# Kernel optimization log

Measured on AMD Instinct MI355X. Metric: run time of the kernel, lower is better.

Reference implementation:

```python
import jax, jax.numpy as jnp
import numpy as np

B, Q, DIM, HEADS, HEAD_DIM, KV = 32, 4, 2048, 16, 128, 8192


def setup_inputs() -> dict:
    key = jax.random.key(0)
    ks = jax.random.split(key, 9)
    s = 0.02
    return {
        'x': jax.random.normal(ks[0], (B, Q, DIM), jnp.float32),
        'attn_bias': jax.random.normal(ks[1], (B, HEADS, Q, KV), jnp.float32),
        'cache_k': jax.random.normal(ks[2], (B, KV, HEAD_DIM), jnp.float32),
        'cache_v': jax.random.normal(ks[3], (B, KV, HEAD_DIM), jnp.float32),
        'wq': jax.random.normal(ks[4], (DIM, HEADS, HEAD_DIM), jnp.float32) * s,
        'bq': jnp.zeros((HEADS, HEAD_DIM), jnp.float32),
        'wk': jax.random.normal(ks[5], (DIM, HEAD_DIM), jnp.float32) * s,
        'bk': jnp.zeros((HEAD_DIM,), jnp.float32),
        'wv': jax.random.normal(ks[6], (DIM, HEAD_DIM), jnp.float32) * s,
        'bv': jnp.zeros((HEAD_DIM,), jnp.float32),
        'wo': jax.random.normal(ks[7], (HEADS, HEAD_DIM, DIM), jnp.float32) * s,
        'bo': jnp.zeros((DIM,), jnp.float32),
    }


def reference(x, attn_bias, cache_k, cache_v, wq, bq, wk, bk, wv, bv, wo, bo):
    q_len = x.shape[1]
    # projections (MQA: shared single-head K/V)
    q = jnp.einsum('bqd,dhe->bqhe', x, wq) + bq          # [B,Q,H,hd]
    k_new = x @ wk + bk                                   # [B,Q,hd]
    v_new = x @ wv + bv
    # rolling KV cache update: shift left by q_len, write new tokens at end
    k = jnp.roll(cache_k, -q_len, axis=1).at[:, -q_len:].set(k_new)  # [B,KV,hd]
    v = jnp.roll(cache_v, -q_len, axis=1).at[:, -q_len:].set(v_new)
    scale = 1.0 / (k.shape[-1] ** 0.5)
    p = jnp.einsum('bqhe,bke->bhqk', q, k) * scale        # [B,H,Q,KV]
    a = jax.nn.softmax(p + attn_bias, axis=-1)
    o = jnp.einsum('bhqk,bke->bqhe', a, v)                # [B,Q,H,hd]
    return jnp.einsum('bqhe,hed->bqd', o, wo) + bo        # [B,Q,DIM]
```

## Files before the change

### kernel.cpp

```cpp
#include <hip/hip_runtime.h>
#include <cstddef>
#include <cstdint>

#define BATCH 32
#define QL 4
#define DIM 2048
#define NH 16
#define HD 128
#define KVLEN 8192
#define HQ 64
#define CHUNK 256
#define NCKB 32
#define NCK 16
#define KT 64
#define NT 4

typedef __attribute__((ext_vector_type(8))) short bf16x8;
typedef __attribute__((ext_vector_type(4))) float f32x4;

__device__ __forceinline__ unsigned short cvt_bf16(float f) {
    unsigned int u = __builtin_bit_cast(unsigned int, f);
    u += 0x7fffu + ((u >> 16) & 1u);
    return (unsigned short)(u >> 16);
}
__device__ __forceinline__ unsigned int pack2(float a, float b) {
    return (unsigned int)cvt_bf16(a) | ((unsigned int)cvt_bf16(b) << 16);
}
__device__ __forceinline__ float bf16_to_f32(unsigned short s) {
    unsigned int u = ((unsigned int)s) << 16;
    return __builtin_bit_cast(float, u);
}
__device__ __forceinline__ bf16x8 mk_frag(unsigned int a, unsigned int b,
                                          unsigned int c, unsigned int d) {
    unsigned int t[4] = {a, b, c, d};
    return *(const bf16x8*)t;
}

template<int VARIANT>
__global__ __launch_bounds__(256) void gemm_kernel(
    const float* __restrict__ A,
    const float* __restrict__ w0p, const float* __restrict__ w1p,
    const float* __restrict__ w2p,
    const float* __restrict__ b0p, const float* __restrict__ b1p,
    const float* __restrict__ b2p,
    float* __restrict__ o0, float* __restrict__ o1, float* __restrict__ o2)
{
    const int n0 = blockIdx.x * 64;
    const int m0 = blockIdx.y * 64;
    const int kz = blockIdx.z * 256;
    const int tid = threadIdx.x;
    const int wave = tid >> 6, lane = tid & 63;
    const int l15 = lane & 15, quad = lane >> 4;

    const float* W; const float* Bv; int ldw, nc;
    if (VARIANT == 0) {
        if (n0 >= 2176)      { W = w2p; Bv = b2p; ldw = 128;  nc = n0 - 2176; }
        else if (n0 >= 2048) { W = w1p; Bv = b1p; ldw = 128;  nc = n0 - 2048; }
        else                 { W = w0p; Bv = b0p; ldw = 2048; nc = n0; }
    } else { W = w0p; Bv = b0p; ldw = 2048; nc = n0; }

    __shared__ alignas(16) unsigned short a_s[64][72];
    __shared__ alignas(16) unsigned short w_s[64][68];

    const int wn = tid & 63;
    const int wk0 = (tid >> 6) * 4;

    f32x4 acc[4];
    #pragma unroll
    for (int nt = 0; nt < 4; ++nt) acc[nt] = (f32x4){0.f, 0.f, 0.f, 0.f};

    float4 apre[4];
    float wpre[4][4];

    #pragma unroll
    for (int ii = 0; ii < 4; ++ii) {
        int f = tid + 256 * ii, r = f >> 4, c4 = (f & 15) << 2;
        apre[ii] = *(const float4*)&A[(size_t)(m0 + r) * DIM + kz + c4];
    }
    #pragma unroll
    for (int sub = 0; sub < 4; ++sub) {
        int k0 = kz + wk0 + 16 * sub;
        const float* wp = W + (size_t)k0 * ldw + nc + wn;
        #pragma unroll
        for (int j = 0; j < 4; ++j) wpre[sub][j] = wp[(size_t)j * ldw];
    }

    for (int it = 0; it < 4; ++it) {
        __syncthreads();
        #pragma unroll
        for (int ii = 0; ii < 4; ++ii) {
            int f = tid + 256 * ii, r = f >> 4, c4 = (f & 15) << 2;
            *(uint2*)&a_s[r][c4] =
                make_uint2(pack2(apre[ii].x, apre[ii].y), pack2(apre[ii].z, apre[ii].w));
        }
        #pragma unroll
        for (int sub = 0; sub < 4; ++sub) {
            int k0 = wk0 + 16 * sub;
            *(uint2*)&w_s[wn][k0] =
                make_uint2(pack2(wpre[sub][0], wpre[sub][1]),
                           pack2(wpre[sub][2], wpre[sub][3]));
        }
        __syncthreads();
        if (it + 1 < 4) {
            const int kb = kz + (it + 1) * 64;
            #pragma unroll
            for (int ii = 0; ii < 4; ++ii) {
                int f = tid + 256 * ii, r = f >> 4, c4 = (f & 15) << 2;
                apre[ii] = *(const float4*)&A[(size_t)(m0 + r) * DIM + kb + c4];
            }
            #pragma unroll
            for (int sub = 0; sub < 4; ++sub) {
                int k0 = kb + wk0 + 16 * sub;
                const float* wp = W + (size_t)k0 * ldw + nc + wn;
                #pragma unroll
                for (int j = 0; j < 4; ++j) wpre[sub][j] = wp[(size_t)j * ldw];
            }
        }
        #pragma unroll
        for (int kf = 0; kf < 2; ++kf) {
            bf16x8 af = *(const bf16x8*)&a_s[16 * wave + l15][kf * 32 + quad * 8];
            #pragma unroll
            for (int nt = 0; nt < 4; ++nt) {
                uint2 lo = *(const uint2*)&w_s[nt * 16 + l15][kf * 32 + quad * 8];
                uint2 hi = *(const uint2*)&w_s[nt * 16 + l15][kf * 32 + quad * 8 + 4];
                bf16x8 wf = mk_frag(lo.x, lo.y, hi.x, hi.y);
                acc[nt] = __builtin_amdgcn_mfma_f32_16x16x32_bf16(af, wf, acc[nt], 0, 0, 0);
            }
        }
    }
    const bool addb = (blockIdx.z == 0);
    #pragma unroll
    for (int nt = 0; nt < 4; ++nt)
        #pragma unroll
        for (int reg = 0; reg < 4; ++reg) {
            int row = m0 + 16 * wave + quad * 4 + reg;
            int col = n0 + nt * 16 + l15;
            float s = acc[nt][reg];
            if (VARIANT == 1) {
                atomicAdd(&o0[(size_t)row * DIM + col], s + (addb ? Bv[col] : 0.f));
            } else {
                int b = row >> 2, q = row & 3;
                if (col < 2048) {
                    int h = col >> 7, e = col & 127;
                    atomicAdd(&o0[((size_t)(b * 64 + h * 4 + q)) * 128 + e],
                              s + (addb ? b0p[col] : 0.f));
                } else if (col < 2176) {
                    int e = col - 2048;
                    atomicAdd(&o1[(size_t)row * 128 + e], s + (addb ? b1p[e] : 0.f));
                } else {
                    int e = col - 2176;
                    atomicAdd(&o2[(size_t)row * 128 + e], s + (addb ? b2p[e] : 0.f));
                }
            }
        }
}

__global__ __launch_bounds__(256, 2) void attn_kernel(
    const float* __restrict__ qws, const float* __restrict__ kws,
    const float* __restrict__ vws,
    const float* __restrict__ cachek, const float* __restrict__ cachev,
    const float* __restrict__ abias,
    float* __restrict__ opart, float* __restrict__ lpart)
{
    const int ck = blockIdx.x;
    const int b  = blockIdx.y;
    const int tid = threadIdx.x;
    const int wave = tid >> 6, lane = tid & 63;
    const int l15 = lane & 15, quad = lane >> 4;
    const float scale = 0.08838834764831845f;

    __shared__ alignas(16) unsigned short k_s[KT][136];
    __shared__ alignas(16) unsigned short v_sT[HD][68];
    __shared__ alignas(16) unsigned short p_s[4][16][72];

    bf16x8 qf[4];
    {
        const float* qrow = qws + ((size_t)b * HQ + 16 * wave + l15) * HD;
        #pragma unroll
        for (int kf = 0; kf < 4; ++kf) {
            float4 f0 = *(const float4*)&qrow[kf * 32 + quad * 8];
            float4 f1 = *(const float4*)&qrow[kf * 32 + quad * 8 + 4];
            qf[kf] = mk_frag(pack2(f0.x, f0.y), pack2(f0.z, f0.w),
                             pack2(f1.x, f1.y), pack2(f1.z, f1.w));
        }
    }

    const int kbase0 = ck * CHUNK;
    const int ve = tid & 127;
    const int vkq = (tid >> 7);

    const float* bptr[4];
    #pragma unroll
    for (int reg = 0; reg < 4; ++reg) {
        int hq = 16 * wave + quad * 4 + reg;
        int h = hq >> 2, q = hq & 3;
        bptr[reg] = abias + (((size_t)(b * NH + h)) * QL + q) * KVLEN + kbase0 + l15;
    }

    float4 kpre[8];
    float vpre[8][4];
    float bpre[16];

    #pragma unroll
    for (int i = 0; i < 8; ++i) {
        int f = tid + 256 * i;
        int row = f >> 5, e0 = (f & 31) << 2;
        int kv = kbase0 + row;
        const float* pk = (kv < KVLEN - QL)
            ? cachek + ((size_t)b * KVLEN + kv + QL) * HD + e0
            : kws + ((size_t)b * QL + (kv - (KVLEN - QL))) * HD + e0;
        kpre[i] = *(const float4*)pk;
    }
    #pragma unroll
    for (int i = 0; i < 8; ++i) {
        int kv0 = kbase0 + (vkq + 2 * i) * 4;
        #pragma unroll
        for (int j = 0; j < 4; ++j) {
            int kv = kv0 + j;
            const float* pv = (kv < KVLEN - QL)
                ? cachev + ((size_t)b * KVLEN + kv + QL) * HD + ve
                : vws + ((size_t)b * QL + (kv - (KVLEN - QL))) * HD + ve;
            vpre[i][j] = *pv;
        }
    }
    #pragma unroll
    for (int nt = 0; nt < 4; ++nt)
        #pragma unroll
        for (int reg = 0; reg < 4; ++reg)
            bpre[nt * 4 + reg] = bptr[reg][nt * 16];

    f32x4 oa[8];
    #pragma unroll
    for (int n8 = 0; n8 < 8; ++n8) oa[n8] = (f32x4){0.f, 0.f, 0.f, 0.f};
    float lrow[4] = {0.f, 0.f, 0.f, 0.f};

    for (int t = 0; t < NT; ++t) {
        __syncthreads();
        #pragma unroll
        for (int i = 0; i < 8; ++i) {
            int f = tid + 256 * i;
            int row = f >> 5, e0 = (f & 31) << 2;
            *(uint2*)&k_s[row][e0] =
                make_uint2(pack2(kpre[i].x, kpre[i].y), pack2(kpre[i].z, kpre[i].w));
        }
        #pragma unroll
        for (int i = 0; i < 8; ++i) {
            int kv0 = (vkq + 2 * i) * 4;
            *(uint2*)&v_sT[ve][kv0] =
                make_uint2(pack2(vpre[i][0], vpre[i][1]),
                           pack2(vpre[i][2], vpre[i][3]));
        }
        float bias[16];
        #pragma unroll
        for (int j = 0; j < 16; ++j) bias[j] = bpre[j];
        __syncthreads();
        if (t + 1 < NT) {
            const int tb = kbase0 + (t + 1) * KT;
            #pragma unroll
            for (int i = 0; i < 8; ++i) {
                int f = tid + 256 * i;
                int row = f >> 5, e0 = (f & 31) << 2;
                int kv = tb + row;
                const float* pk = (kv < KVLEN - QL)
                    ? cachek + ((size_t)b * KVLEN + kv + QL) * HD + e0
                    : kws + ((size_t)b * QL + (kv - (KVLEN - QL))) * HD + e0;
                kpre[i] = *(const float4*)pk;
            }
            #pragma unroll
            for (int i = 0; i < 8; ++i) {
                int kv0 = tb + (vkq + 2 * i) * 4;
                #pragma unroll
                for (int j = 0; j < 4; ++j) {
                    int kv = kv0 + j;
                    const float* pv = (kv < KVLEN - QL)
                        ? cachev + ((size_t)b * KVLEN + kv + QL) * HD + ve
                        : vws + ((size_t)b * QL + (kv - (KVLEN - QL))) * HD + ve;
                    vpre[i][j] = *pv;
                }
            }
            #pragma unroll
            for (int nt = 0; nt < 4; ++nt)
                #pragma unroll
                for (int reg = 0; reg < 4; ++reg)
                    bpre[nt * 4 + reg] = bptr[reg][(t + 1) * KT + nt * 16];
        }
        f32x4 sacc[4];
        #pragma unroll
        for (int nt = 0; nt < 4; ++nt) sacc[nt] = (f32x4){0.f, 0.f, 0.f, 0.f};
        #pragma unroll
        for (int kf = 0; kf < 4; ++kf) {
            #pragma unroll
            for (int nt = 0; nt < 4; ++nt) {
                bf16x8 kfb = *(const bf16x8*)&k_s[nt * 16 + l15][kf * 32 + quad * 8];
                sacc[nt] = __builtin_amdgcn_mfma_f32_16x16x32_bf16(qf[kf], kfb, sacc[nt], 0, 0, 0);
            }
        }
        #pragma unroll
        for (int nt = 0; nt < 4; ++nt)
            #pragma unroll
            for (int reg = 0; reg < 4; ++reg) {
                float s = sacc[nt][reg] * scale + bias[nt * 4 + reg];
                float p = __expf(s);
                unsigned short pb = cvt_bf16(p);
                lrow[reg] += bf16_to_f32(pb);
                p_s[wave][quad * 4 + reg][nt * 16 + l15] = pb;
            }
        #pragma unroll
        for (int kfp = 0; kfp < 2; ++kfp) {
            uint2 plo = *(const uint2*)&p_s[wave][l15][kfp * 32 + quad * 8];
            uint2 phi = *(const uint2*)&p_s[wave][l15][kfp * 32 + quad * 8 + 4];
            bf16x8 pf = mk_frag(plo.x, plo.y, phi.x, phi.y);
            #pragma unroll
            for (int n8 = 0; n8 < 8; ++n8) {
                uint2 vlo = *(const uint2*)&v_sT[n8 * 16 + l15][kfp * 32 + quad * 8];
                uint2 vhi = *(const uint2*)&v_sT[n8 * 16 + l15][kfp * 32 + quad * 8 + 4];
                bf16x8 vf = mk_frag(vlo.x, vlo.y, vhi.x, vhi.y);
                oa[n8] = __builtin_amdgcn_mfma_f32_16x16x32_bf16(pf, vf, oa[n8], 0, 0, 0);
            }
        }
    }
    #pragma unroll
    for (int reg = 0; reg < 4; ++reg) {
        float v = lrow[reg];
        v += __shfl_xor(v, 1);
        v += __shfl_xor(v, 2);
        v += __shfl_xor(v, 4);
        v += __shfl_xor(v, 8);
        lrow[reg] = v;
    }
    const size_t slot = (size_t)(b * NCK + (ck >> 1));
    const size_t obase = slot * HQ * HD;
    #pragma unroll
    for (int n8 = 0; n8 < 8; ++n8)
        #pragma unroll
        for (int reg = 0; reg < 4; ++reg) {
            int hq = 16 * wave + quad * 4 + reg;
            int e = n8 * 16 + l15;
            atomicAdd(&opart[obase + (size_t)hq * HD + e], oa[n8][reg]);
        }
    if (l15 == 0) {
        #pragma unroll
        for (int reg = 0; reg < 4; ++reg) {
            int hq = 16 * wave + quad * 4 + reg;
            atomicAdd(&lpart[slot * HQ + hq], lrow[reg]);
        }
    }
}

__global__ __launch_bounds__(128) void combine_kernel(
    const float* __restrict__ opart, const float* __restrict__ lpart,
    float* __restrict__ ored)
{
    const int bh = blockIdx.x;
    const int b = bh >> 6, hq = bh & 63;
    const int e = threadIdx.x;
    float lt = 0.f, ov = 0.f;
    #pragma unroll
    for (int c = 0; c < NCK; ++c) {
        lt += lpart[(b * NCK + c) * HQ + hq];
        ov += opart[((size_t)(b * NCK + c) * HQ + hq) * HD + e];
    }
    int h = hq >> 2, q = hq & 3;
    ored[(size_t)(b * QL + q) * DIM + h * HD + e] = ov / lt;
}

extern "C" void kernel_launch(void* const* d_in, const int* in_sizes, int n_in,
                              void* d_out, int out_size, void* d_ws, size_t ws_size,
                              hipStream_t stream)
{
    const float* x   = (const float*)d_in[0];
    const float* ab  = (const float*)d_in[1];
    const float* cK  = (const float*)d_in[2];
    const float* cV  = (const float*)d_in[3];
    const float* wq  = (const float*)d_in[4];
    const float* bq  = (const float*)d_in[5];
    const float* wk  = (const float*)d_in[6];
    const float* bk  = (const float*)d_in[7];
    const float* wv  = (const float*)d_in[8];
    const float* bv  = (const float*)d_in[9];
    const float* wo  = (const float*)d_in[10];
    const float* bo  = (const float*)d_in[11];
    float* out = (float*)d_out;

    float* ws   = (float*)d_ws;
    float* wsq  = ws;
    float* wsk  = wsq + 262144;
    float* wsv  = wsk + 16384;
    float* wsop = wsv + 16384;
    float* wsl  = wsop + 4194304;
    float* wsor = wsl + 32768;

    hipMemsetAsync(wsq,  0, (size_t)(262144 + 16384 + 16384) * sizeof(float), stream);
    hipMemsetAsync(wsop, 0, (size_t)(4194304 + 32768) * sizeof(float), stream);
    hipMemsetAsync(out,  0, (size_t)(BATCH * QL * DIM) * sizeof(float), stream);

    gemm_kernel<0><<<dim3(36, 2, 8), 256, 0, stream>>>(
        x, wq, wk, wv, bq, bk, bv, wsq, wsk, wsv);
    attn_kernel<<<dim3(NCKB, BATCH), 256, 0, stream>>>(
        wsq, wsk, wsv, cK, cV, ab, wsop, wsl);
    combine_kernel<<<BATCH * HQ, 128, 0, stream>>>(wsop, wsl, wsor);
    gemm_kernel<1><<<dim3(32, 2, 8), 256, 0, stream>>>(
        wsor, wo, nullptr, nullptr, bo, nullptr, nullptr, out, nullptr, nullptr);
}
```

Measured before the change: 402.6 us.

## Load K fragments directly from global, drop K LDS staging, merge memsets

The attention kernel no longer stages K tiles through shared memory with register prefetch. Each lane now reads its K fragment straight from global memory into MFMA operands, and the bias is read directly instead of being prefetched. This cuts LDS footprint and register pressure, so launch bounds are raised to 4 blocks per SM. In exchange, K loads are no longer overlapped with compute and are not shared across waves, so each of the four waves reloads the same K rows. The three memsets are merged into one contiguous workspace memset, and zeroing of the output moves into the combine kernel.

Result: slower. 448.5 us (+11.4%).

```diff
diff --git a/kernel.cpp b/kernel.cpp
--- a/kernel.cpp
+++ b/kernel.cpp
@@ -155,7 +155,7 @@
         }
 }
 
-__global__ __launch_bounds__(256, 2) void attn_kernel(
+__global__ __launch_bounds__(256, 4) void attn_kernel(
     const float* __restrict__ qws, const float* __restrict__ kws,
     const float* __restrict__ vws,
     const float* __restrict__ cachek, const float* __restrict__ cachev,
@@ -169,7 +169,6 @@
     const int l15 = lane & 15, quad = lane >> 4;
     const float scale = 0.08838834764831845f;
 
-    __shared__ alignas(16) unsigned short k_s[KT][136];
     __shared__ alignas(16) unsigned short v_sT[HD][68];
     __shared__ alignas(16) unsigned short p_s[4][16][72];
 
@@ -197,20 +196,8 @@
         bptr[reg] = abias + (((size_t)(b * NH + h)) * QL + q) * KVLEN + kbase0 + l15;
     }
 
-    float4 kpre[8];
     float vpre[8][4];
-    float bpre[16];
-
-    #pragma unroll
-    for (int i = 0; i < 8; ++i) {
-        int f = tid + 256 * i;
-        int row = f >> 5, e0 = (f & 31) << 2;
-        int kv = kbase0 + row;
-        const float* pk = (kv < KVLEN - QL)
-            ? cachek + ((size_t)b * KVLEN + kv + QL) * HD + e0
-            : kws + ((size_t)b * QL + (kv - (KVLEN - QL))) * HD + e0;
-        kpre[i] = *(const float4*)pk;
-    }
+
     #pragma unroll
     for (int i = 0; i < 8; ++i) {
         int kv0 = kbase0 + (vkq + 2 * i) * 4;
@@ -223,11 +210,6 @@
             vpre[i][j] = *pv;
         }
     }
-    #pragma unroll
-    for (int nt = 0; nt < 4; ++nt)
-        #pragma unroll
-        for (int reg = 0; reg < 4; ++reg)
-            bpre[nt * 4 + reg] = bptr[reg][nt * 16];
 
     f32x4 oa[8];
     #pragma unroll
@@ -236,13 +218,6 @@
 
     for (int t = 0; t < NT; ++t) {
         __syncthreads();
-        #pragma unroll
-        for (int i = 0; i < 8; ++i) {
-            int f = tid + 256 * i;
-            int row = f >> 5, e0 = (f & 31) << 2;
-            *(uint2*)&k_s[row][e0] =
-                make_uint2(pack2(kpre[i].x, kpre[i].y), pack2(kpre[i].z, kpre[i].w));
-        }
         #pragma unroll
         for (int i = 0; i < 8; ++i) {
             int kv0 = (vkq + 2 * i) * 4;
@@ -250,22 +225,9 @@
                 make_uint2(pack2(vpre[i][0], vpre[i][1]),
                            pack2(vpre[i][2], vpre[i][3]));
         }
-        float bias[16];
-        #pragma unroll
-        for (int j = 0; j < 16; ++j) bias[j] = bpre[j];
         __syncthreads();
         if (t + 1 < NT) {
             const int tb = kbase0 + (t + 1) * KT;
-            #pragma unroll
-            for (int i = 0; i < 8; ++i) {
-                int f = tid + 256 * i;
-                int row = f >> 5, e0 = (f & 31) << 2;
-                int kv = tb + row;
-                const float* pk = (kv < KVLEN - QL)
-                    ? cachek + ((size_t)b * KVLEN + kv + QL) * HD + e0
-                    : kws + ((size_t)b * QL + (kv - (KVLEN - QL))) * HD + e0;
-                kpre[i] = *(const float4*)pk;
-            }
             #pragma unroll
             for (int i = 0; i < 8; ++i) {
                 int kv0 = tb + (vkq + 2 * i) * 4;
@@ -278,11 +240,15 @@
                     vpre[i][j] = *pv;
                 }
             }
-            #pragma unroll
-            for (int nt = 0; nt < 4; ++nt)
-                #pragma unroll
-                for (int reg = 0; reg < 4; ++reg)
-                    bpre[nt * 4 + reg] = bptr[reg][(t + 1) * KT + nt * 16];
+        }
+        const int tb0 = kbase0 + t * KT;
+        const float* kp[4];
+        #pragma unroll
+        for (int nt = 0; nt < 4; ++nt) {
+            int kv = tb0 + nt * 16 + l15;
+            kp[nt] = (kv < KVLEN - QL)
+                ? cachek + ((size_t)b * KVLEN + kv + QL) * HD
+                : kws + ((size_t)b * QL + (kv - (KVLEN - QL))) * HD;
         }
         f32x4 sacc[4];
         #pragma unroll
@@ -291,7 +257,10 @@
         for (int kf = 0; kf < 4; ++kf) {
             #pragma unroll
             for (int nt = 0; nt < 4; ++nt) {
-                bf16x8 kfb = *(const bf16x8*)&k_s[nt * 16 + l15][kf * 32 + quad * 8];
+                float4 f0 = *(const float4*)(kp[nt] + kf * 32 + quad * 8);
+                float4 f1 = *(const float4*)(kp[nt] + kf * 32 + quad * 8 + 4);
+                bf16x8 kfb = mk_frag(pack2(f0.x, f0.y), pack2(f0.z, f0.w),
+                                     pack2(f1.x, f1.y), pack2(f1.z, f1.w));
                 sacc[nt] = __builtin_amdgcn_mfma_f32_16x16x32_bf16(qf[kf], kfb, sacc[nt], 0, 0, 0);
             }
         }
@@ -299,7 +268,7 @@
         for (int nt = 0; nt < 4; ++nt)
             #pragma unroll
             for (int reg = 0; reg < 4; ++reg) {
-                float s = sacc[nt][reg] * scale + bias[nt * 4 + reg];
+                float s = sacc[nt][reg] * scale + bptr[reg][t * KT + nt * 16];
                 float p = __expf(s);
                 unsigned short pb = cvt_bf16(p);
                 lrow[reg] += bf16_to_f32(pb);
@@ -349,11 +318,12 @@
 
 __global__ __launch_bounds__(128) void combine_kernel(
     const float* __restrict__ opart, const float* __restrict__ lpart,
-    float* __restrict__ ored)
+    float* __restrict__ ored, float* __restrict__ outz)
 {
     const int bh = blockIdx.x;
     const int b = bh >> 6, hq = bh & 63;
     const int e = threadIdx.x;
+    outz[(size_t)bh * 128 + e] = 0.f;
     float lt = 0.f, ov = 0.f;
     #pragma unroll
     for (int c = 0; c < NCK; ++c) {
@@ -390,15 +360,15 @@
     float* wsl  = wsop + 4194304;
     float* wsor = wsl + 32768;
 
-    hipMemsetAsync(wsq,  0, (size_t)(262144 + 16384 + 16384) * sizeof(float), stream);
-    hipMemsetAsync(wsop, 0, (size_t)(4194304 + 32768) * sizeof(float), stream);
-    hipMemsetAsync(out,  0, (size_t)(BATCH * QL * DIM) * sizeof(float), stream);
+    hipMemsetAsync(ws, 0,
+        (size_t)(262144 + 16384 + 16384 + 4194304 + 32768) * sizeof(float),
+        stream);
 
     gemm_kernel<0><<<dim3(36, 2, 8), 256, 0, stream>>>(
         x, wq, wk, wv, bq, bk, bv, wsq, wsk, wsv);
     attn_kernel<<<dim3(NCKB, BATCH), 256, 0, stream>>>(
         wsq, wsk, wsv, cK, cV, ab, wsop, wsl);
-    combine_kernel<<<BATCH * HQ, 128, 0, stream>>>(wsop, wsl, wsor);
+    combine_kernel<<<BATCH * HQ, 128, 0, stream>>>(wsop, wsl, wsor, out);
     gemm_kernel<1><<<dim3(32, 2, 8), 256, 0, stream>>>(
         wsor, wo, nullptr, nullptr, bo, nullptr, nullptr, out, nullptr, nullptr);
 }
```
